# Kernel optimization log

Hardware: AMD Instinct MI355X
Metric: run time of the kernel (lower is better)

Reference implementation:

```python
import jax, jax.numpy as jnp
import numpy as np

B, N, E, H = 4, 4096, 256, 1024
N_W = int(np.ceil(np.log2(N)))        # 12 chord layers
N_LINKS = N_W + 1                      # 13 links per row (self + 2^k offsets)


def _chord_cols(n_vec, n_link):
    # cols[i] = [i, (i+2^0)%N, (i+2^1)%N, ..., (i+2^(n_link-2))%N]
    offs = np.concatenate([[0], 2 ** np.arange(n_link - 1)])
    return ((np.arange(n_vec)[:, None] + offs[None, :]) % n_vec).astype(np.int32)


def setup_inputs() -> dict:
    key = jax.random.key(0)
    ks = jax.random.split(key, 12)
    s = 0.02
    inp = {
        "V": jax.random.normal(ks[0], (B, N, E), jnp.float32),
        "input": jax.random.normal(ks[1], (B, N, E), jnp.float32),
        # g MLP: Linear(E,H) -> GELU -> Linear(H,E)
        "g_W1": jax.random.normal(ks[2], (E, H), jnp.float32) * s,
        "g_b1": jnp.zeros((H,), jnp.float32),
        "g_W2": jax.random.normal(ks[3], (H, E), jnp.float32) * s,
        "g_b2": jnp.zeros((E,), jnp.float32),
        # fs MLPs (stacked over n_W layers): Linear(E,H) -> GELU -> Linear(H,n_links)
        "f_W1": jax.random.normal(ks[4], (N_W, E, H), jnp.float32) * s,
        "f_b1": jnp.zeros((N_W, H), jnp.float32),
        "f_W2": jax.random.normal(ks[5], (N_W, H, N_LINKS), jnp.float32) * s,
        "f_b2": jnp.zeros((N_W, N_LINKS), jnp.float32),
        "cols": jnp.asarray(_chord_cols(N, N_LINKS)),  # [N, n_links] int32
    }
    return inp


def _gelu(x):
    return jax.nn.gelu(x, approximate=False)  # torch nn.GELU default (erf)


def reference(V, input, g_W1, g_b1, g_W2, g_b2, f_W1, f_b1, f_W2, f_b2, cols):
    # V = g(V)
    V = _gelu(jnp.einsum('bne,eh->bnh', V, g_W1) + g_b1)
    V = jnp.einsum('bnh,he->bne', V, g_W2) + g_b2
    n_w = f_W1.shape[0]
    for m in range(n_w):  # fixed small layer loop
        res = V
        # W = fs[m](input) -> per-row chord edge weights [B, N, n_links]
        Wh = _gelu(jnp.einsum('bne,eh->bnh', input, f_W1[m]) + f_b1[m])
        W = jnp.einsum('bnh,hl->bnl', Wh, f_W2[m]) + f_b2[m]
        # structured sparse spmm: row i aggregates cols[i] with weights W[:, i, :]
        Vg = V[:, cols, :]                     # [B, N, n_links, E] gather
        V = jnp.einsum('bnl,bnle->bne', W, Vg) + res
    # dropout is identity in eval / drop_prob=0
    return V
```

## Files before the change

### kernel.cpp

```cpp
#include <hip/hip_runtime.h>
#include <hip/hip_bf16.h>
#include <hip/hip_fp16.h>
#include <math.h>

#define BB 4
#define NN 4096
#define EE 256
#define HH 1024
#define NW 12
#define NL 13
#define MM (BB * NN)

typedef __attribute__((ext_vector_type(8))) short short8;
typedef __attribute__((ext_vector_type(4))) float f32x4;
typedef __attribute__((ext_vector_type(2))) _Float16 h2;
typedef __attribute__((ext_vector_type(8))) _Float16 half8;

__device__ __forceinline__ float gelu_fast(float x) {
    float t = __builtin_fmaf(0.044715f, x * x, 1.0f);
    float e = __builtin_amdgcn_exp2f(-2.3021193f * (x * t));
    return x * __builtin_amdgcn_rcpf(1.0f + e);
}

__device__ __forceinline__ unsigned gelu2_f16(float a, float b) {
    const h2 C1 = {(_Float16)-2.3021193f, (_Float16)-2.3021193f};
    const h2 C2 = {(_Float16)0.044715f, (_Float16)0.044715f};
    const h2 ONE = {(_Float16)1.0f, (_Float16)1.0f};
    h2 x;
    asm("v_cvt_pkrtz_f16_f32 %0, %1, %2" : "=v"(x) : "v"(a), "v"(b));
    h2 x2 = x * x;
    h2 t  = C2 * x2 + ONE;
    h2 z  = (C1 * x) * t;
    __half2 es = h2exp2(__builtin_bit_cast(__half2, z));
    h2 d = ONE + __builtin_bit_cast(h2, es);
    __half2 rs = h2rcp(__builtin_bit_cast(__half2, d));
    h2 y = x * __builtin_bit_cast(h2, rs);
    return __builtin_bit_cast(unsigned, y);
}

__device__ __forceinline__ h2 cvt_pk_f16(float a, float b) {
    h2 r;
    asm("v_cvt_pkrtz_f16_f32 %0, %1, %2" : "=v"(r) : "v"(a), "v"(b));
    return r;
}

__device__ __forceinline__ unsigned cvt_pk_bf16(float a, float b) {
    unsigned r;
    asm("v_cvt_pk_bf16_f32 %0, %1, %2" : "=v"(r) : "v"(a), "v"(b));
    return r;
}

__device__ __forceinline__ void load_lds16(const void* g, void* l) {
    __builtin_amdgcn_global_load_lds(
        (const __attribute__((address_space(1))) void*)g,
        (__attribute__((address_space(3))) void*)l, 16, 0, 0);
}

__global__ __launch_bounds__(256) void gemm2_bn64(
    const __hip_bfloat16* __restrict__ A,
    const __hip_bfloat16* __restrict__ Bt,
    const float* __restrict__ bias,
    _Float16* __restrict__ C)
{
    __shared__ __hip_bfloat16 As[128 * 32];
    __shared__ __hip_bfloat16 Bs[64 * 32];

    const int tid = threadIdx.x;
    const int w = tid >> 6, l = tid & 63;
    const int wr = w >> 1, wc = w & 1;
    const int row0 = blockIdx.y * 128;
    const int col0 = blockIdx.x * 64;

    const int c0 = w * 64 + l;
    const int c1 = c0 + 256;
    const __hip_bfloat16* gA0 = A  + (size_t)(row0 + (c0 >> 2)) * HH + (c0 & 3) * 8;
    const __hip_bfloat16* gA1 = A  + (size_t)(row0 + (c1 >> 2)) * HH + (c1 & 3) * 8;
    const __hip_bfloat16* gB0 = Bt + (size_t)(col0 + (c0 >> 2)) * HH + (c0 & 3) * 8;
    char* dA0 = (char*)As + c0 * 16;
    char* dA1 = (char*)As + c1 * 16;
    char* dB0 = (char*)Bs + c0 * 16;

    const int lr = l & 15;
    const int lk = (l >> 4) * 8;

    f32x4 acc[4][2] = {};

    for (int k0 = 0; k0 < HH; k0 += 32) {
        load_lds16(gA0 + k0, dA0);
        load_lds16(gA1 + k0, dA1);
        load_lds16(gB0 + k0, dB0);
        __syncthreads();

        short8 a[4], b[2];
        #pragma unroll
        for (int m = 0; m < 4; ++m)
            a[m] = *(const short8*)&As[(wr * 64 + m * 16 + lr) * 32 + lk];
        #pragma unroll
        for (int n = 0; n < 2; ++n)
            b[n] = *(const short8*)&Bs[(wc * 32 + n * 16 + lr) * 32 + lk];
        #pragma unroll
        for (int m = 0; m < 4; ++m)
            #pragma unroll
            for (int n = 0; n < 2; ++n)
                acc[m][n] = __builtin_amdgcn_mfma_f32_16x16x32_bf16(a[m], b[n], acc[m][n], 0, 0, 0);
        __syncthreads();
    }

    #pragma unroll
    for (int m = 0; m < 4; ++m) {
        #pragma unroll
        for (int n = 0; n < 2; ++n) {
            const int col = col0 + wc * 32 + n * 16 + lr;
            const float bv = bias[col];
            #pragma unroll
            for (int j = 0; j < 4; ++j) {
                const int row = row0 + wr * 64 + m * 16 + (l >> 4) * 4 + j;
                C[(size_t)row * EE + col] = (_Float16)(acc[m][n][j] + bv);
            }
        }
    }
}

__global__ __launch_bounds__(256, 3) void gemm1_areg(
    const __hip_bfloat16* __restrict__ A,
    const __hip_bfloat16* __restrict__ W1t,
    const float* __restrict__ b1,
    __hip_bfloat16* __restrict__ Wh)
{
    __shared__ __hip_bfloat16 Bs[8 * 64 * 32];
    __shared__ __align__(16) char Gb[4][4096];

    const int tid = threadIdx.x;
    const int w = tid >> 6, l = tid & 63;
    const int row0 = blockIdx.x * 128;
    const int col0 = blockIdx.y * 128;
    const int lr = l & 15, g = l >> 4, lk = g * 8;

    short8 xf[2][8];
    {
        const __hip_bfloat16* xp0 = A + (size_t)(row0 + w * 32 + lr) * EE + lk;
        #pragma unroll
        for (int kk = 0; kk < 8; ++kk) {
            xf[0][kk] = *(const short8*)(xp0 + kk * 32);
            xf[1][kk] = *(const short8*)(xp0 + 16 * EE + kk * 32);
        }
    }
    char* Gw = Gb[w];

    #pragma unroll
    for (int rstep = 0; rstep < 8; ++rstep) {
        const int c = rstep * 256 + tid;
        load_lds16(W1t + (size_t)(col0 + ((c >> 2) & 63)) * EE + (c >> 8) * 32 + (c & 3) * 8,
                   (char*)Bs + c * 16);
    }
    __syncthreads();

    #pragma unroll 1
    for (int ct = 0; ct < 2; ++ct) {
        f32x4 acc[4][2];
        #pragma unroll
        for (int ni = 0; ni < 4; ++ni) {
            const float4 bv = *(const float4*)&b1[col0 + ct * 64 + ni * 16 + g * 4];
            const f32x4 bi = {bv.x, bv.y, bv.z, bv.w};
            acc[ni][0] = bi;
            acc[ni][1] = bi;
        }
        __builtin_amdgcn_s_setprio(1);
        #pragma unroll
        for (int kk = 0; kk < 8; ++kk) {
            short8 a[4];
            #pragma unroll
            for (int ni = 0; ni < 4; ++ni)
                a[ni] = *(const short8*)((const char*)Bs +
                         (kk * 4096 + ni * 1024 + lr * 64 + g * 16));
            #pragma unroll
            for (int ni = 0; ni < 4; ++ni) {
                acc[ni][0] = __builtin_amdgcn_mfma_f32_16x16x32_bf16(a[ni], xf[0][kk], acc[ni][0], 0, 0, 0);
                acc[ni][1] = __builtin_amdgcn_mfma_f32_16x16x32_bf16(a[ni], xf[1][kk], acc[ni][1], 0, 0, 0);
            }
        }
        __builtin_amdgcn_s_setprio(0);
        __syncthreads();

        if (ct == 0) {
            #pragma unroll
            for (int rstep = 0; rstep < 8; ++rstep) {
                const int c = rstep * 256 + tid;
                load_lds16(W1t + (size_t)(col0 + 64 + ((c >> 2) & 63)) * EE + (c >> 8) * 32 + (c & 3) * 8,
                           (char*)Bs + c * 16);
            }
        }

        #pragma unroll
        for (int ni = 0; ni < 4; ++ni) {
            #pragma unroll
            for (int mi = 0; mi < 2; ++mi) {
                const int rloc = mi * 16 + lr;
                const float v0 = gelu_fast(acc[ni][mi][0]);
                const float v1 = gelu_fast(acc[ni][mi][1]);
                const float v2 = gelu_fast(acc[ni][mi][2]);
                const float v3 = gelu_fast(acc[ni][mi][3]);
                uint2 pk;
                pk.x = cvt_pk_bf16(v0, v1);
                pk.y = cvt_pk_bf16(v2, v3);
                const int byte = (rloc * 128 + (ni * 16 + g * 4) * 2) ^ ((rloc & 7) << 4);
                *(uint2*)(Gw + byte) = pk;
            }
        }

        #pragma unroll
        for (int p = 0; p < 4; ++p) {
            const int rl = p * 8 + (l >> 3);
            const int hb = (l & 7) * 16;
            const uint4 v = *(const uint4*)(Gw + ((rl * 128 + hb) ^ ((rl & 7) << 4)));
            *(uint4*)((char*)(Wh + (size_t)(row0 + w * 32 + rl) * HH + col0 + ct * 64) + hb) = v;
        }
        __syncthreads();
    }
}

__global__ __launch_bounds__(256, 3) void f_fused(
    const __hip_bfloat16* __restrict__ X,
    const __hip_bfloat16* __restrict__ W1t,
    const float* __restrict__ b1,
    const _Float16* __restrict__ W2t,
    const float* __restrict__ b2,
    float* __restrict__ Wall_t)
{
    __shared__ __hip_bfloat16 Bs[8 * 64 * 32];
    __shared__ __align__(16) char Gb[4][4096];
    __shared__ float biasS[HH];

    const int tid = threadIdx.x;
    const int w = tid >> 6, l = tid & 63;
    const int row0 = blockIdx.x * 128;
    const int m_lv = blockIdx.y;
    const int lr = l & 15;
    const int g  = l >> 4;
    const int lk = g * 8;

    const __hip_bfloat16* W1m = W1t + (size_t)m_lv * HH * EE;

    ((float4*)biasS)[tid] = ((const float4*)(b1 + (size_t)m_lv * HH))[tid];

    short8 xf[2][8];
    {
        const __hip_bfloat16* xp0 = X + (size_t)(row0 + w * 32 + lr) * EE + lk;
        #pragma unroll
        for (int kk = 0; kk < 8; ++kk) {
            xf[0][kk] = *(const short8*)(xp0 + kk * 32);
            xf[1][kk] = *(const short8*)(xp0 + 16 * EE + kk * 32);
        }
    }

    const _Float16* w2p = W2t + ((size_t)m_lv * 16 + lr) * HH + lk;
    char* Gw = Gb[w];

    f32x4 wacc0 = {}, wacc1 = {};

    #pragma unroll
    for (int rstep = 0; rstep < 8; ++rstep) {
        const int c = rstep * 256 + tid;
        load_lds16(W1m + (size_t)((c >> 2) & 63) * EE + (c >> 8) * 32 + (c & 3) * 8,
                   (char*)Bs + c * 16);
    }
    __syncthreads();

    #pragma unroll 1
    for (int ct = 0; ct < 16; ++ct) {
        f32x4 acc[4][2];
        #pragma unroll
        for (int ni = 0; ni < 4; ++ni) {
            const float4 bv = *(const float4*)&biasS[ct * 64 + ni * 16 + g * 4];
            const f32x4 bi = {bv.x, bv.y, bv.z, bv.w};
            acc[ni][0] = bi;
            acc[ni][1] = bi;
        }
        __builtin_amdgcn_s_setprio(1);
        #pragma unroll
        for (int kk = 0; kk < 8; ++kk) {
            short8 a[4];
            #pragma unroll
            for (int ni = 0; ni < 4; ++ni)
                a[ni] = *(const short8*)((const char*)Bs +
                         (kk * 4096 + ni * 1024 + lr * 64 + g * 16));
            #pragma unroll
            for (int ni = 0; ni < 4; ++ni) {
                acc[ni][0] = __builtin_amdgcn_mfma_f32_16x16x32_bf16(a[ni], xf[0][kk], acc[ni][0], 0, 0, 0);
                acc[ni][1] = __builtin_amdgcn_mfma_f32_16x16x32_bf16(a[ni], xf[1][kk], acc[ni][1], 0, 0, 0);
            }
        }
        __builtin_amdgcn_s_setprio(0);
        __syncthreads();

        if (ct < 15) {
            const __hip_bfloat16* W1n = W1m + (size_t)(ct + 1) * 64 * EE;
            #pragma unroll
            for (int rstep = 0; rstep < 8; ++rstep) {
                const int c = rstep * 256 + tid;
                load_lds16(W1n + (size_t)((c >> 2) & 63) * EE + (c >> 8) * 32 + (c & 3) * 8,
                           (char*)Bs + c * 16);
            }
        }

        #pragma unroll
        for (int ni = 0; ni < 4; ++ni) {
            #pragma unroll
            for (int mi = 0; mi < 2; ++mi) {
                const int rloc = mi * 16 + lr;
                uint2 pk;
                pk.x = gelu2_f16(acc[ni][mi][0], acc[ni][mi][1]);
                pk.y = gelu2_f16(acc[ni][mi][2], acc[ni][mi][3]);
                const int byte = (rloc * 128 + (ni * 16 + g * 4) * 2) ^ ((rloc & 7) << 4);
                *(uint2*)(Gw + byte) = pk;
            }
        }

        #pragma unroll
        for (int ks2 = 0; ks2 < 2; ++ks2) {
            const half8 aw = *(const half8*)(w2p + ct * 64 + ks2 * 32);
            {
                const int byte = (lr * 128 + (ks2 * 32 + lk) * 2) ^ ((lr & 7) << 4);
                const half8 bg = *(const half8*)(Gw + byte);
                wacc0 = __builtin_amdgcn_mfma_f32_16x16x32_f16(aw, bg, wacc0, 0, 0, 0);
            }
            {
                const int rloc = 16 + lr;
                const int byte = (rloc * 128 + (ks2 * 32 + lk) * 2) ^ ((rloc & 7) << 4);
                const half8 bg = *(const half8*)(Gw + byte);
                wacc1 = __builtin_amdgcn_mfma_f32_16x16x32_f16(aw, bg, wacc1, 0, 0, 0);
            }
        }
        __syncthreads();
    }

    const float* b2m = b2 + m_lv * NL;
    #pragma unroll
    for (int j = 0; j < 4; ++j) {
        const int lval = g * 4 + j;
        const float bv = (lval < NL) ? b2m[lval] : 0.f;
        float* wp = Wall_t + (size_t)(m_lv * 16 + lval) * MM;
        wp[row0 + w * 32 + lr]      = wacc0[j] + bv;
        wp[row0 + w * 32 + 16 + lr] = wacc1[j] + bv;
    }
}

struct bf4 { __hip_bfloat16 a, b, c, d; };

__device__ __forceinline__ void cvt_body(
    const float* __restrict__ in, __hip_bfloat16* __restrict__ out, int i)
{
    float4 v = ((const float4*)in)[i];
    bf4 o;
    o.a = __float2bfloat16(v.x); o.b = __float2bfloat16(v.y);
    o.c = __float2bfloat16(v.z); o.d = __float2bfloat16(v.w);
    ((bf4*)out)[i] = o;
}

__device__ __forceinline__ void transpose_body(
    const float* __restrict__ inB, __hip_bfloat16* __restrict__ outB,
    int K, int N, int bx, int by, float (*t)[33])
{
    const int n0 = bx * 32, k0 = by * 32;
    const int tx = threadIdx.x & 31, ty = threadIdx.x >> 5;
    #pragma unroll
    for (int i = 0; i < 32; i += 8)
        t[ty + i][tx] = inB[(size_t)(k0 + ty + i) * N + n0 + tx];
    __syncthreads();
    #pragma unroll
    for (int i = 0; i < 32; i += 8)
        outB[(size_t)(n0 + ty + i) * K + k0 + tx] = __float2bfloat16(t[tx][ty + i]);
}

__global__ __launch_bounds__(256) void prep_all(
    const float* __restrict__ V, const float* __restrict__ input,
    const float* __restrict__ g_W1, const float* __restrict__ g_W2,
    const float* __restrict__ f_W1, const float* __restrict__ f_W2,
    __hip_bfloat16* __restrict__ Vb, __hip_bfloat16* __restrict__ Xb,
    __hip_bfloat16* __restrict__ gW1t, __hip_bfloat16* __restrict__ gW2t,
    __hip_bfloat16* __restrict__ fW1t, _Float16* __restrict__ W2tA)
{
    __shared__ float t[32][33];
    const int bid = blockIdx.x;
    const int tid = threadIdx.x;

    if (bid < 4096) {
        cvt_body(V, Vb, bid * 256 + tid);
    } else if (bid < 8192) {
        cvt_body(input, Xb, (bid - 4096) * 256 + tid);
    } else if (bid < 8448) {
        const int b2 = bid - 8192;
        transpose_body(g_W1, gW1t, EE, HH, b2 & 31, b2 >> 5, t);
    } else if (bid < 8704) {
        const int b2 = bid - 8448;
        transpose_body(g_W2, gW2t, HH, EE, b2 & 7, b2 >> 3, t);
    } else if (bid < 11776) {
        const int b2 = bid - 8704;
        const int z = b2 >> 8, r = b2 & 255;
        transpose_body(f_W1 + (size_t)z * EE * HH, fW1t + (size_t)z * HH * EE,
                       EE, HH, r & 31, r >> 5, t);
    } else {
        const int idx = (bid - 11776) * 256 + tid;
        const int m = idx >> 14;
        const int n = (idx >> 10) & 15;
        const int h = idx & 1023;
        const float v = (n < NL) ? f_W2[((size_t)m * HH + h) * NL + n] : 0.f;
        W2tA[idx] = (_Float16)v;
    }
}

__global__ __launch_bounds__(1024, 1) void chord_lds(
    const uint2* __restrict__ Vg,
    const float* __restrict__ Wall_t,
    float4* __restrict__ outF)
{
    __shared__ unsigned L[2][2][NN];

    const int tid = threadIdx.x;
    const int bid = blockIdx.x;
    const int batch = bid >> 6;
    const int slice = bid & 63;
    const int gbase = batch * NN;

    #pragma unroll
    for (int i = 0; i < 4; ++i) {
        const int n = tid + i * 1024;
        const uint2 u = Vg[(size_t)(gbase + n) * 64 + slice];
        L[0][0][n] = u.x;
        L[0][1][n] = u.y;
    }
    __syncthreads();

    int cur = 0;
    #pragma unroll 1
    for (int m = 0; m < NW; ++m) {
        const float* wbase = Wall_t + (size_t)m * 16 * MM + gbase;
        const int nxt = cur ^ 1;
        #pragma unroll 1
        for (int i = 0; i < 4; ++i) {
            const int n = tid + i * 1024;
            h2 a01 = __builtin_bit_cast(h2, L[cur][0][n]);
            h2 a23 = __builtin_bit_cast(h2, L[cur][1][n]);
            #pragma unroll
            for (int l = 0; l < NL; ++l) {
                const int off = (l == 0) ? 0 : (1 << (l - 1));
                const int cn = (n + off) & (NN - 1);
                const float wv = wbase[(size_t)l * MM + n];
                const h2 w2 = cvt_pk_f16(wv, wv);
                const h2 x01 = __builtin_bit_cast(h2, L[cur][0][cn]);
                const h2 x23 = __builtin_bit_cast(h2, L[cur][1][cn]);
                a01 = w2 * x01 + a01;
                a23 = w2 * x23 + a23;
            }
            if (m == NW - 1) {
                float4 o = {(float)a01[0], (float)a01[1],
                            (float)a23[0], (float)a23[1]};
                outF[(size_t)(gbase + n) * 64 + slice] = o;
            } else {
                L[nxt][0][n] = __builtin_bit_cast(unsigned, a01);
                L[nxt][1][n] = __builtin_bit_cast(unsigned, a23);
            }
        }
        __syncthreads();
        cur ^= 1;
    }
}

extern "C" void kernel_launch(void* const* d_in, const int* in_sizes, int n_in,
                              void* d_out, int out_size, void* d_ws, size_t ws_size,
                              hipStream_t stream)
{
    const float* V      = (const float*)d_in[0];
    const float* input  = (const float*)d_in[1];
    const float* g_W1   = (const float*)d_in[2];
    const float* g_b1   = (const float*)d_in[3];
    const float* g_W2   = (const float*)d_in[4];
    const float* g_b2   = (const float*)d_in[5];
    const float* f_W1   = (const float*)d_in[6];
    const float* f_b1   = (const float*)d_in[7];
    const float* f_W2   = (const float*)d_in[8];
    const float* f_b2   = (const float*)d_in[9];
    float* out = (float*)d_out;

    char* ws = (char*)d_ws;
    size_t o = 0;
    __hip_bfloat16* Vb     = (__hip_bfloat16*)(ws + o); o += (size_t)MM * EE * 2;
    __hip_bfloat16* Xb     = (__hip_bfloat16*)(ws + o); o += (size_t)MM * EE * 2;
    __hip_bfloat16* gW1t   = (__hip_bfloat16*)(ws + o); o += (size_t)HH * EE * 2;
    __hip_bfloat16* gW2t   = (__hip_bfloat16*)(ws + o); o += (size_t)EE * HH * 2;
    __hip_bfloat16* fW1t   = (__hip_bfloat16*)(ws + o); o += (size_t)NW * HH * EE * 2;
    _Float16*       W2tA   = (_Float16*)(ws + o);       o += (size_t)NW * 16 * HH * 2;
    __hip_bfloat16* Whb    = (__hip_bfloat16*)(ws + o); o += (size_t)MM * HH * 2;
    float*          Wall   = (float*)(ws + o);          o += (size_t)NW * 16 * MM * 4;
    _Float16*       Vg0    = (_Float16*)(ws + o);       o += (size_t)MM * EE * 2;

    dim3 blk(256);

    prep_all<<<12544, blk, 0, stream>>>(V, input, g_W1, g_W2, f_W1, f_W2,
                                        Vb, Xb, gW1t, gW2t, fW1t, W2tA);

    gemm1_areg<<<dim3(MM / 128, HH / 128), blk, 0, stream>>>(Vb, gW1t, g_b1, Whb);
    gemm2_bn64<<<dim3(EE / 64, MM / 128), blk, 0, stream>>>(Whb, gW2t, g_b2, Vg0);

    f_fused<<<dim3(MM / 128, NW), blk, 0, stream>>>(Xb, fW1t, f_b1, W2tA, f_b2, Wall);

    chord_lds<<<256, dim3(1024), 0, stream>>>((const uint2*)Vg0, Wall, (float4*)out);
}
```

Measured before the change: 250.7 us.

## Use 32x32x16 MFMA in f_fused and pre-pack chord weights as f16 pairs

The first GEMM in f_fused switches from 16x16x32 bf16 MFMAs to 32x32x16 bf16 MFMAs. This reorganises the register-resident X fragments, the bias initialisation and the GELU writeback indexing to match the new accumulator layout, and is meant to cut LDS operand reads and instruction count per FLOP. The edge-weight output is now written already converted to packed f16 pairs, so chord_lds no longer does a conversion per weight load. The buffer stays 4 bytes per element, so traffic is unchanged. The risk is that the new MFMA lane mapping is mismatched with the swizzled Gb layout.

```diff
diff --git a/kernel.cpp b/kernel.cpp
--- a/kernel.cpp
+++ b/kernel.cpp
@@ -13,6 +13,7 @@
 
 typedef __attribute__((ext_vector_type(8))) short short8;
 typedef __attribute__((ext_vector_type(4))) float f32x4;
+typedef __attribute__((ext_vector_type(16))) float f32x16;
 typedef __attribute__((ext_vector_type(2))) _Float16 h2;
 typedef __attribute__((ext_vector_type(8))) _Float16 half8;
 
@@ -225,7 +226,7 @@
     const float* __restrict__ b1,
     const _Float16* __restrict__ W2t,
     const float* __restrict__ b2,
-    float* __restrict__ Wall_t)
+    unsigned* __restrict__ Wall_u)
 {
     __shared__ __hip_bfloat16 Bs[8 * 64 * 32];
     __shared__ __align__(16) char Gb[4][4096];
@@ -238,19 +239,19 @@
     const int lr = l & 15;
     const int g  = l >> 4;
     const int lk = g * 8;
+    const int lr32 = l & 31;
+    const int h8   = l >> 5;
 
     const __hip_bfloat16* W1m = W1t + (size_t)m_lv * HH * EE;
 
     ((float4*)biasS)[tid] = ((const float4*)(b1 + (size_t)m_lv * HH))[tid];
 
-    short8 xf[2][8];
+    short8 xf[16];
     {
-        const __hip_bfloat16* xp0 = X + (size_t)(row0 + w * 32 + lr) * EE + lk;
-        #pragma unroll
-        for (int kk = 0; kk < 8; ++kk) {
-            xf[0][kk] = *(const short8*)(xp0 + kk * 32);
-            xf[1][kk] = *(const short8*)(xp0 + 16 * EE + kk * 32);
-        }
+        const __hip_bfloat16* xp = X + (size_t)(row0 + w * 32 + lr32) * EE + h8 * 8;
+        #pragma unroll
+        for (int ks = 0; ks < 16; ++ks)
+            xf[ks] = *(const short8*)(xp + ks * 16);
     }
 
     const _Float16* w2p = W2t + ((size_t)m_lv * 16 + lr) * HH + lk;
@@ -268,26 +269,30 @@
 
     #pragma unroll 1
     for (int ct = 0; ct < 16; ++ct) {
-        f32x4 acc[4][2];
-        #pragma unroll
-        for (int ni = 0; ni < 4; ++ni) {
-            const float4 bv = *(const float4*)&biasS[ct * 64 + ni * 16 + g * 4];
-            const f32x4 bi = {bv.x, bv.y, bv.z, bv.w};
-            acc[ni][0] = bi;
-            acc[ni][1] = bi;
+        f32x16 acc[2];
+        #pragma unroll
+        for (int ht = 0; ht < 2; ++ht) {
+            #pragma unroll
+            for (int q = 0; q < 4; ++q) {
+                const float4 bv = *(const float4*)&biasS[ct * 64 + ht * 32 + q * 8 + h8 * 4];
+                acc[ht][q * 4 + 0] = bv.x;
+                acc[ht][q * 4 + 1] = bv.y;
+                acc[ht][q * 4 + 2] = bv.z;
+                acc[ht][q * 4 + 3] = bv.w;
+            }
         }
         __builtin_amdgcn_s_setprio(1);
         #pragma unroll
         for (int kk = 0; kk < 8; ++kk) {
-            short8 a[4];
-            #pragma unroll
-            for (int ni = 0; ni < 4; ++ni)
-                a[ni] = *(const short8*)((const char*)Bs +
-                         (kk * 4096 + ni * 1024 + lr * 64 + g * 16));
-            #pragma unroll
-            for (int ni = 0; ni < 4; ++ni) {
-                acc[ni][0] = __builtin_amdgcn_mfma_f32_16x16x32_bf16(a[ni], xf[0][kk], acc[ni][0], 0, 0, 0);
-                acc[ni][1] = __builtin_amdgcn_mfma_f32_16x16x32_bf16(a[ni], xf[1][kk], acc[ni][1], 0, 0, 0);
+            #pragma unroll
+            for (int t = 0; t < 2; ++t) {
+                const int ks = kk * 2 + t;
+                #pragma unroll
+                for (int ht = 0; ht < 2; ++ht) {
+                    const short8 a = *(const short8*)((const char*)Bs +
+                        (kk * 4096 + (ht * 32 + lr32) * 64 + t * 32 + h8 * 16));
+                    acc[ht] = __builtin_amdgcn_mfma_f32_32x32x16_bf16(a, xf[ks], acc[ht], 0, 0, 0);
+                }
             }
         }
         __builtin_amdgcn_s_setprio(0);
@@ -304,14 +309,14 @@
         }
 
         #pragma unroll
-        for (int ni = 0; ni < 4; ++ni) {
-            #pragma unroll
-            for (int mi = 0; mi < 2; ++mi) {
-                const int rloc = mi * 16 + lr;
+        for (int ht = 0; ht < 2; ++ht) {
+            #pragma unroll
+            for (int q = 0; q < 4; ++q) {
+                const int h = ht * 32 + q * 8 + h8 * 4;
                 uint2 pk;
-                pk.x = gelu2_f16(acc[ni][mi][0], acc[ni][mi][1]);
-                pk.y = gelu2_f16(acc[ni][mi][2], acc[ni][mi][3]);
-                const int byte = (rloc * 128 + (ni * 16 + g * 4) * 2) ^ ((rloc & 7) << 4);
+                pk.x = gelu2_f16(acc[ht][q * 4 + 0], acc[ht][q * 4 + 1]);
+                pk.y = gelu2_f16(acc[ht][q * 4 + 2], acc[ht][q * 4 + 3]);
+                const int byte = (lr32 * 128 + h * 2) ^ ((lr32 & 7) << 4);
                 *(uint2*)(Gw + byte) = pk;
             }
         }
@@ -339,9 +344,11 @@
     for (int j = 0; j < 4; ++j) {
         const int lval = g * 4 + j;
         const float bv = (lval < NL) ? b2m[lval] : 0.f;
-        float* wp = Wall_t + (size_t)(m_lv * 16 + lval) * MM;
-        wp[row0 + w * 32 + lr]      = wacc0[j] + bv;
-        wp[row0 + w * 32 + 16 + lr] = wacc1[j] + bv;
+        unsigned* wp = Wall_u + (size_t)(m_lv * 16 + lval) * MM;
+        const float v0 = wacc0[j] + bv;
+        const float v1 = wacc1[j] + bv;
+        wp[row0 + w * 32 + lr]      = __builtin_bit_cast(unsigned, cvt_pk_f16(v0, v0));
+        wp[row0 + w * 32 + 16 + lr] = __builtin_bit_cast(unsigned, cvt_pk_f16(v1, v1));
     }
 }
 
@@ -411,7 +418,7 @@
 
 __global__ __launch_bounds__(1024, 1) void chord_lds(
     const uint2* __restrict__ Vg,
-    const float* __restrict__ Wall_t,
+    const unsigned* __restrict__ Wall_u,
     float4* __restrict__ outF)
 {
     __shared__ unsigned L[2][2][NN];
@@ -434,7 +441,7 @@
     int cur = 0;
     #pragma unroll 1
     for (int m = 0; m < NW; ++m) {
-        const float* wbase = Wall_t + (size_t)m * 16 * MM + gbase;
+        const unsigned* wbase = Wall_u + (size_t)m * 16 * MM + gbase;
         const int nxt = cur ^ 1;
         #pragma unroll 1
         for (int i = 0; i < 4; ++i) {
@@ -445,8 +452,7 @@
             for (int l = 0; l < NL; ++l) {
                 const int off = (l == 0) ? 0 : (1 << (l - 1));
                 const int cn = (n + off) & (NN - 1);
-                const float wv = wbase[(size_t)l * MM + n];
-                const h2 w2 = cvt_pk_f16(wv, wv);
+                const h2 w2 = __builtin_bit_cast(h2, wbase[(size_t)l * MM + n]);
                 const h2 x01 = __builtin_bit_cast(h2, L[cur][0][cn]);
                 const h2 x23 = __builtin_bit_cast(h2, L[cur][1][cn]);
                 a01 = w2 * x01 + a01;
@@ -491,7 +497,7 @@
     __hip_bfloat16* fW1t   = (__hip_bfloat16*)(ws + o); o += (size_t)NW * HH * EE * 2;
     _Float16*       W2tA   = (_Float16*)(ws + o);       o += (size_t)NW * 16 * HH * 2;
     __hip_bfloat16* Whb    = (__hip_bfloat16*)(ws + o); o += (size_t)MM * HH * 2;
-    float*          Wall   = (float*)(ws + o);          o += (size_t)NW * 16 * MM * 4;
+    unsigned*       Wall   = (unsigned*)(ws + o);       o += (size_t)NW * 16 * MM * 4;
     _Float16*       Vg0    = (_Float16*)(ws + o);       o += (size_t)MM * EE * 2;
 
     dim3 blk(256);
```

After: 263.0 us. 4.9% more time.
